# Optimization experiments

Hardware: AMD Instinct MI355X
Metric: run time of the kernel (lower is better)

The kernel has to match this reference:

```python
import math
import jax, jax.numpy as jnp
import numpy as np

BASE = 10000.0
SCALING_FACTOR = 1.0
ORIG_MAX_POS = 4096
BETA_FAST, BETA_SLOW = 32, 1
MSCALE = 0.707
MSCALE_ALL_DIM = 0.707


def _yarn_cos_sin(seq_len: int, dim: int):
    # DeepseekV3YarnRotaryEmbedding._set_cos_sin_cache, computed in numpy (constants)
    def corr_dim(num_rot):
        return dim * math.log(ORIG_MAX_POS / (num_rot * 2 * math.pi)) / (2 * math.log(BASE))
    low = max(math.floor(corr_dim(BETA_FAST)), 0)
    high = min(math.ceil(corr_dim(BETA_SLOW)), dim - 1)
    hi = high + 0.001 if low == high else high
    ramp = np.clip((np.arange(dim // 2, dtype=np.float32) - low) / (hi - low), 0.0, 1.0)
    inv_freq_mask = 1.0 - ramp
    freq_extra = 1.0 / BASE ** (np.arange(0, dim, 2, dtype=np.float32) / dim)
    freq_inter = freq_extra / SCALING_FACTOR
    inv_freq = freq_inter * (1.0 - inv_freq_mask) + freq_extra * inv_freq_mask
    t = np.arange(seq_len, dtype=np.float32)
    freqs = np.outer(t, inv_freq)
    def get_mscale(s, m):
        return 1.0 if s <= 1 else 0.1 * m * math.log(s) + 1.0
    _m = get_mscale(SCALING_FACTOR, MSCALE) / get_mscale(SCALING_FACTOR, MSCALE_ALL_DIM)
    emb = np.concatenate([freqs, freqs], axis=-1)  # [S, dim]
    return jnp.asarray(np.cos(emb) * _m), jnp.asarray(np.sin(emb) * _m)


def _rotate_half(x):
    x1, x2 = jnp.split(x, 2, axis=-1)
    return jnp.concatenate([-x2, x1], axis=-1)


def setup_inputs() -> dict:
    key = jax.random.key(0)
    ks = jax.random.split(key, 5)
    B, S, H, DN, DR, DV = 2, 2048, 16, 128, 64, 128
    return {
        "q_nope": jax.random.normal(ks[0], (B, S, H, DN), jnp.float32),
        "q_pe": jax.random.normal(ks[1], (B, S, H, DR), jnp.float32),
        "k_nope": jax.random.normal(ks[2], (B, S, H, DN), jnp.float32),
        "k_pe": jax.random.normal(ks[3], (B, S, 1, DR), jnp.float32),  # shared rope key head
        "v": jax.random.normal(ks[4], (B, S, H, DV), jnp.float32),
    }


def reference(q_nope, q_pe, k_nope, k_pe, v):
    B, S, H, DN = q_nope.shape
    DR = q_pe.shape[-1]
    sm_scale = (DN + DR) ** (-0.5)  # qk_head_dim**-0.5
    cos, sin = _yarn_cos_sin(S, DR)  # [S, DR]
    cos = cos[None, :, None, :]
    sin = sin[None, :, None, :]
    # decoupled RoPE on the rope slice (apply_rotary_pos_emb with position_ids=arange)
    qp = q_pe * cos + _rotate_half(q_pe) * sin              # [B,S,H,DR]
    kp = k_pe * cos + _rotate_half(k_pe) * sin              # [B,S,1,DR]
    kp = jnp.broadcast_to(kp, (B, S, H, DR))
    q = jnp.concatenate([q_nope, qp], axis=-1)              # [B,S,H,DN+DR]
    k = jnp.concatenate([k_nope, kp], axis=-1)
    # attention_ref: full fp32 logits, causal mask, lse*log2(e), softmax, PV
    logits = jnp.einsum('bmhd,bnhd->bhmn', q.astype(jnp.float32), k.astype(jnp.float32)) * sm_scale
    mask = jnp.arange(S)[:, None] >= jnp.arange(S)[None, :]  # qo_len == kv_len
    logits = jnp.where(mask[None, None], logits, -jnp.inf)
    lse = jnp.transpose(jax.scipy.special.logsumexp(logits, axis=-1), (0, 2, 1)) * math.log2(math.e)
    p = jax.nn.softmax(logits, axis=-1)
    o = jnp.einsum('bhmn,bnhd->bmhd', p, v.astype(jnp.float32))
    o = o.reshape(B * S, H, -1).astype(q_nope.dtype)        # [B*S, H, DV]
    return o, lse
```

## Files before the change

kernel.cpp:

```cpp
#include <hip/hip_runtime.h>
#include <hip/hip_bf16.h>
#include <math.h>

#define NB 2
#define SEQ 2048
#define NH 16
#define DNOPE 128
#define DROT 64
#define DVDIM 128
#define DQK 192
#define BM 64
#define BN 64

typedef __bf16 bf16x8_t __attribute__((ext_vector_type(8)));
typedef float f32x4_t __attribute__((ext_vector_type(4)));

#define LOG2_BASE_OVER_HALFDIM 0.41524101186092028f
#define KSL2 0.10412340175817158f
#define INV_2PI 0.15915494309189535f

typedef __attribute__((address_space(1))) unsigned int as1_uint;
typedef __attribute__((address_space(3))) unsigned int as3_uint;
#define GLOAD16(g, l)                                                        \
  __builtin_amdgcn_global_load_lds((as1_uint*)(g), (as3_uint*)(l), 16, 0, 0)

#define KBF_ELEMS   ((size_t)NB * NH * SEQ * DQK)

#define KN_BLOCKS 4096
#define KR_BLOCKS 128
#define VPREP_BLOCKS 1024

__global__ __launch_bounds__(256) void prep_kernel(
    const float* __restrict__ k_nope, const float* __restrict__ k_pe,
    const float* __restrict__ v, __bf16* __restrict__ Kbf,
    __bf16* __restrict__ Vtb) {
  __shared__ __bf16 T[64][130];
  const int bid = blockIdx.x;
  const int tid = threadIdx.x;
  if (bid < KN_BLOCKS) {
    int gid = bid * 256 + tid;
    int d0 = (gid & 15) * 8;
    int rest = gid >> 4;
    int s = (rest >> 4) & (SEQ - 1);
    int h = rest & (NH - 1);
    int b = rest >> 15;
    const float* p = k_nope + ((size_t)((b * SEQ + s) * NH + h)) * DNOPE + d0;
    float4 a = *(const float4*)p;
    float4 c = *(const float4*)(p + 4);
    bf16x8_t o;
    o[0] = (__bf16)a.x; o[1] = (__bf16)a.y; o[2] = (__bf16)a.z; o[3] = (__bf16)a.w;
    o[4] = (__bf16)c.x; o[5] = (__bf16)c.y; o[6] = (__bf16)c.z; o[7] = (__bf16)c.w;
    *(bf16x8_t*)&Kbf[((size_t)(b * NH + h) * SEQ + s) * DQK + d0] = o;
  } else if (bid < KN_BLOCKS + KR_BLOCKS) {
    int gid = (bid - KN_BLOCKS) * 256 + tid;
    int dr0 = (gid & 7) * 8;
    int rest = gid >> 3;
    int s = rest & (SEQ - 1);
    int b = rest >> 11;
    const float* p = k_pe + (size_t)(b * SEQ + s) * DROT;
    float4 x0 = *(const float4*)(p + dr0);
    float4 x1 = *(const float4*)(p + dr0 + 4);
    int dro = (dr0 < 32) ? dr0 + 32 : dr0 - 32;
    float4 y0 = *(const float4*)(p + dro);
    float4 y1 = *(const float4*)(p + dro + 4);
    float sgn = (dr0 < 32) ? -1.0f : 1.0f;
    float xs[8] = {x0.x, x0.y, x0.z, x0.w, x1.x, x1.y, x1.z, x1.w};
    float ys[8] = {y0.x, y0.y, y0.z, y0.w, y1.x, y1.y, y1.z, y1.w};
    float invf0 = exp2f(-LOG2_BASE_OVER_HALFDIM * (float)(dr0 & 31));
    const float kj[8] = {
      1.0f,
      0.7499083907567589f,
      0.5624875938672282f,
      0.4219181499736729f,
      0.3163923045408737f,
      0.2372497216250197f,
      0.1779391804261401f,
      0.1334543036472316f};
    bf16x8_t o;
#pragma unroll
    for (int j = 0; j < 8; ++j) {
      float rev = (float)s * invf0 * (kj[j] * INV_2PI);
      rev = rev - floorf(rev);
      float sn = __builtin_amdgcn_sinf(rev);
      float cs = __builtin_amdgcn_cosf(rev);
      o[j] = (__bf16)(xs[j] * cs + sgn * ys[j] * sn);
    }
#pragma unroll
    for (int h = 0; h < NH; ++h)
      *(bf16x8_t*)&Kbf[((size_t)(b * NH + h) * SEQ + s) * DQK + DNOPE + dr0] = o;
  } else {
    int vb = bid - KN_BLOCKS - KR_BLOCKS;
    const int s0 = (vb & 31) * 64, h = (vb >> 5) & (NH - 1), b = vb >> 9;
#pragma unroll
    for (int r = 0; r < 8; ++r) {
      int task = tid + r * 256;
      int srow = task >> 5, c4 = (task & 31) * 4;
      const float* p = v + ((size_t)((b * SEQ + s0 + srow) * NH + h)) * DVDIM + c4;
      float4 a = *(const float4*)p;
      T[srow][c4 + 0] = (__bf16)a.x; T[srow][c4 + 1] = (__bf16)a.y;
      T[srow][c4 + 2] = (__bf16)a.z; T[srow][c4 + 3] = (__bf16)a.w;
    }
    __syncthreads();
#pragma unroll
    for (int r = 0; r < 4; ++r) {
      int task = tid + r * 256;
      int dv = task >> 3, c8 = (task & 7) * 8;
      bf16x8_t o;
#pragma unroll
      for (int u = 0; u < 8; ++u) o[u] = T[c8 + u][dv];
      *(bf16x8_t*)&Vtb[((size_t)(b * NH + h) * DVDIM + dv) * SEQ + s0 + c8] = o;
    }
  }
}

__global__ __launch_bounds__(256, 2) void mla_fwd_kernel(
    const float* __restrict__ q_nope, const float* __restrict__ q_pe,
    const __bf16* __restrict__ Kbf, const __bf16* __restrict__ Vtb,
    float* __restrict__ out_o, float* __restrict__ out_lse) {
  __shared__ __bf16 Kl[BN * DQK];
  __shared__ __bf16 Vl0[DVDIM * BN];
  __shared__ __bf16 Vl1[DVDIM * BN];
  __shared__ __bf16 Pl[4 * 16 * BN];

  const int bx = blockIdx.x, h = blockIdx.y, b = blockIdx.z;
  const int tid = threadIdx.x;
  const int w = tid >> 6, lane = tid & 63;
  const int col = lane & 15, quad = lane >> 4;
  const int wm = w & 1;
  const int wnd = w >> 1;
  const int swz = col & 7;
  const int e0 = quad ^ swz, e1 = (quad + 4) ^ swz;
  const int wb = w * 512;

  const __bf16 onev = (col == 0) ? (__bf16)1.0f : (__bf16)0.0f;
  bf16x8_t vxf;
#pragma unroll
  for (int u = 0; u < 8; ++u) vxf[u] = onev;

  const __bf16* Kslab = Kbf + (size_t)(b * NH + h) * SEQ * DQK;
  const __bf16* Vslab = Vtb + (size_t)(b * NH + h) * DVDIM * SEQ;

  int kofs[6];
#pragma unroll
  for (int r = 0; r < 6; ++r) {
    int L = r * 256 + tid;
    int n = L / 24, jj = L - n * 24;
    int jsrc = (jj & ~7) | ((jj & 7) ^ (n & 7));
    kofs[r] = n * DQK + jsrc * 8;
  }
  int vofs[4];
#pragma unroll
  for (int r = 0; r < 4; ++r) {
    int L = r * 256 + tid;
    int dv = L >> 3, jj = L & 7;
    vofs[r] = dv * SEQ + (jj ^ (dv & 7)) * 8;
  }

  for (int half = 0; half < 2; ++half) {
    const int qt = half ? bx : (31 - bx);
    const int qb = qt * BM;

    __syncthreads();
#pragma unroll
    for (int r = 0; r < 6; ++r) GLOAD16(Kslab + kofs[r], &Kl[r * 2048 + wb]);
#pragma unroll
    for (int r = 0; r < 4; ++r) GLOAD16(Vslab + vofs[r], &Vl0[r * 2048 + wb]);

    bf16x8_t qf[2][6];
#pragma unroll
    for (int mt = 0; mt < 2; ++mt) {
      const int mrow = qb + wm * 32 + mt * 16 + col;
      const float* qn = q_nope + (size_t)((b * SEQ + mrow) * NH + h) * DNOPE;
      const float* qp = q_pe   + (size_t)((b * SEQ + mrow) * NH + h) * DROT;
#pragma unroll
      for (int c = 0; c < 4; ++c) {
        const float* p = qn + c * 32 + quad * 8;
        float4 a = *(const float4*)p;
        float4 bq = *(const float4*)(p + 4);
        bf16x8_t f;
        f[0]=(__bf16)(a.x*KSL2);  f[1]=(__bf16)(a.y*KSL2);
        f[2]=(__bf16)(a.z*KSL2);  f[3]=(__bf16)(a.w*KSL2);
        f[4]=(__bf16)(bq.x*KSL2); f[5]=(__bf16)(bq.y*KSL2);
        f[6]=(__bf16)(bq.z*KSL2); f[7]=(__bf16)(bq.w*KSL2);
        qf[mt][c] = f;
      }
      {
        const float* plo = qp + quad * 8;
        const float* phi = qp + 32 + quad * 8;
        float4 lo0 = *(const float4*)plo;
        float4 lo1 = *(const float4*)(plo + 4);
        float4 hi0 = *(const float4*)phi;
        float4 hi1 = *(const float4*)(phi + 4);
        float xl[8] = {lo0.x,lo0.y,lo0.z,lo0.w,lo1.x,lo1.y,lo1.z,lo1.w};
        float xh[8] = {hi0.x,hi0.y,hi0.z,hi0.w,hi1.x,hi1.y,hi1.z,hi1.w};
        bf16x8_t f4v, f5v;
#pragma unroll
        for (int j = 0; j < 8; ++j) {
          int i = quad * 8 + j;
          float invf = exp2f(-LOG2_BASE_OVER_HALFDIM * (float)i);
          float rev = (float)mrow * invf * INV_2PI;
          rev = rev - floorf(rev);
          float sn = __builtin_amdgcn_sinf(rev);
          float cs = __builtin_amdgcn_cosf(rev);
          f4v[j] = (__bf16)((xl[j] * cs - xh[j] * sn) * KSL2);
          f5v[j] = (__bf16)((xh[j] * cs + xl[j] * sn) * KSL2);
        }
        qf[mt][4] = f4v; qf[mt][5] = f5v;
      }
    }

    f32x4_t oacc[2][4];
#pragma unroll
    for (int mt = 0; mt < 2; ++mt)
#pragma unroll
      for (int d = 0; d < 4; ++d) oacc[mt][d] = (f32x4_t){0.f, 0.f, 0.f, 0.f};
    f32x4_t lacc[2];
    lacc[0] = (f32x4_t){0.f, 0.f, 0.f, 0.f};
    lacc[1] = (f32x4_t){0.f, 0.f, 0.f, 0.f};

    auto do_iter = [&](int it, const __bf16* Vcur, __bf16* Vnext) {
      __syncthreads();

      f32x4_t sacc[2][2];
#pragma unroll
      for (int mt = 0; mt < 2; ++mt)
#pragma unroll
        for (int nt = 0; nt < 2; ++nt) sacc[mt][nt] = (f32x4_t){0.f, 0.f, 0.f, 0.f};
#pragma unroll
      for (int nt = 0; nt < 2; ++nt) {
        const __bf16* kr = &Kl[(wnd * 32 + nt * 16 + col) * 24 * 8];
        bf16x8_t kf0 = *(const bf16x8_t*)&kr[e0 * 8];
        bf16x8_t kf1 = *(const bf16x8_t*)&kr[e1 * 8];
        bf16x8_t kf2 = *(const bf16x8_t*)&kr[64 + e0 * 8];
        bf16x8_t kf3 = *(const bf16x8_t*)&kr[64 + e1 * 8];
        bf16x8_t kf4 = *(const bf16x8_t*)&kr[128 + e0 * 8];
        bf16x8_t kf5 = *(const bf16x8_t*)&kr[128 + e1 * 8];
#pragma unroll
        for (int mt = 0; mt < 2; ++mt) {
          sacc[mt][nt] = __builtin_amdgcn_mfma_f32_16x16x32_bf16(qf[mt][0], kf0, sacc[mt][nt], 0, 0, 0);
          sacc[mt][nt] = __builtin_amdgcn_mfma_f32_16x16x32_bf16(qf[mt][1], kf1, sacc[mt][nt], 0, 0, 0);
          sacc[mt][nt] = __builtin_amdgcn_mfma_f32_16x16x32_bf16(qf[mt][2], kf2, sacc[mt][nt], 0, 0, 0);
          sacc[mt][nt] = __builtin_amdgcn_mfma_f32_16x16x32_bf16(qf[mt][3], kf3, sacc[mt][nt], 0, 0, 0);
          sacc[mt][nt] = __builtin_amdgcn_mfma_f32_16x16x32_bf16(qf[mt][4], kf4, sacc[mt][nt], 0, 0, 0);
          sacc[mt][nt] = __builtin_amdgcn_mfma_f32_16x16x32_bf16(qf[mt][5], kf5, sacc[mt][nt], 0, 0, 0);
        }
      }

      const bool dg = (it == qt);
#pragma unroll
      for (int mt = 0; mt < 2; ++mt) {
        __bf16* Pr = &Pl[(wm * 2 + mt) * 16 * BN];
#pragma unroll
        for (int nt = 0; nt < 2; ++nt)
#pragma unroll
          for (int r = 0; r < 4; ++r) {
            float pe = exp2f(sacc[mt][nt][r]);
            if (dg) {
              int nn = (it << 6) + wnd * 32 + nt * 16 + col;
              int mm = qb + wm * 32 + mt * 16 + quad * 4 + r;
              if (nn > mm) pe = 0.0f;
            }
            int row = quad * 4 + r;
            int j = wnd * 4 + nt * 2 + (col >> 3);
            Pr[(row * 8 + (j ^ (row & 7))) * 8 + (col & 7)] = (__bf16)pe;
          }
      }
      __syncthreads();

      if (it < qt) {
        const __bf16* Ksrc = Kslab + (size_t)(it + 1) * BN * DQK;
        const __bf16* Vsrc = Vslab + (it + 1) * BN;
#pragma unroll
        for (int r = 0; r < 6; ++r) GLOAD16(Ksrc + kofs[r], &Kl[r * 2048 + wb]);
#pragma unroll
        for (int r = 0; r < 4; ++r) GLOAD16(Vsrc + vofs[r], &Vnext[r * 2048 + wb]);
      }

      bf16x8_t pf0[2], pf1[2];
#pragma unroll
      for (int mt = 0; mt < 2; ++mt) {
        const __bf16* Pr = &Pl[(wm * 2 + mt) * 16 * BN];
        pf0[mt] = *(const bf16x8_t*)&Pr[(col * 8 + e0) * 8];
        pf1[mt] = *(const bf16x8_t*)&Pr[(col * 8 + e1) * 8];
      }
#pragma unroll
      for (int dt = 0; dt < 4; ++dt) {
        const __bf16* vr = &Vcur[((wnd * 4 + dt) * 16 + col) * 64];
        bf16x8_t vf0 = *(const bf16x8_t*)&vr[e0 * 8];
        bf16x8_t vf1 = *(const bf16x8_t*)&vr[e1 * 8];
#pragma unroll
        for (int mt = 0; mt < 2; ++mt) {
          oacc[mt][dt] = __builtin_amdgcn_mfma_f32_16x16x32_bf16(pf0[mt], vf0, oacc[mt][dt], 0, 0, 0);
          oacc[mt][dt] = __builtin_amdgcn_mfma_f32_16x16x32_bf16(pf1[mt], vf1, oacc[mt][dt], 0, 0, 0);
        }
      }
#pragma unroll
      for (int mt = 0; mt < 2; ++mt) {
        lacc[mt] = __builtin_amdgcn_mfma_f32_16x16x32_bf16(pf0[mt], vxf, lacc[mt], 0, 0, 0);
        lacc[mt] = __builtin_amdgcn_mfma_f32_16x16x32_bf16(pf1[mt], vxf, lacc[mt], 0, 0, 0);
      }
    };

    for (int it = 0; it <= qt; it += 2) {
      do_iter(it, Vl0, Vl1);
      if (it + 1 <= qt) do_iter(it + 1, Vl1, Vl0);
    }

    float lr[2][4], inv_l[2][4];
#pragma unroll
    for (int mt = 0; mt < 2; ++mt)
#pragma unroll
      for (int r = 0; r < 4; ++r) {
        lr[mt][r] = __shfl(lacc[mt][r], lane & 48, 64);
        inv_l[mt][r] = 1.0f / lr[mt][r];
      }
#pragma unroll
    for (int mt = 0; mt < 2; ++mt)
#pragma unroll
      for (int dt = 0; dt < 4; ++dt)
#pragma unroll
        for (int r = 0; r < 4; ++r) {
          int mm = qb + wm * 32 + mt * 16 + quad * 4 + r;
          int dd = wnd * 64 + dt * 16 + col;
          out_o[(size_t)((b * SEQ + mm) * NH + h) * DVDIM + dd] =
              oacc[mt][dt][r] * inv_l[mt][r];
        }
    if (wnd == 0 && col < 4) {
#pragma unroll
      for (int mt = 0; mt < 2; ++mt) {
        int mm = qb + wm * 32 + mt * 16 + quad * 4 + col;
        out_lse[(size_t)(b * SEQ + mm) * NH + h] = log2f(lr[mt][col]);
      }
    }
  }
}

extern "C" void kernel_launch(void* const* d_in, const int* in_sizes, int n_in,
                              void* d_out, int out_size, void* d_ws, size_t ws_size,
                              hipStream_t stream) {
  const float* q_nope = (const float*)d_in[0];
  const float* q_pe   = (const float*)d_in[1];
  const float* k_nope = (const float*)d_in[2];
  const float* k_pe   = (const float*)d_in[3];
  const float* v      = (const float*)d_in[4];
  float* out_o   = (float*)d_out;
  float* out_lse = out_o + (size_t)NB * SEQ * NH * DVDIM;

  __bf16* Kbf = (__bf16*)d_ws;
  __bf16* Vtb = Kbf + KBF_ELEMS;

  prep_kernel<<<dim3(KN_BLOCKS + KR_BLOCKS + VPREP_BLOCKS), dim3(256), 0, stream>>>(
      k_nope, k_pe, v, Kbf, Vtb);
  mla_fwd_kernel<<<dim3(16, NH, NB), dim3(256), 0, stream>>>(
      q_nope, q_pe, Kbf, Vtb, out_o, out_lse);
}
```

Measured before the change: 228.3 us.

## Process both causal query tiles concurrently in one 512-thread block sharing K/V loads

Each block now runs 8 waves: four handle the early query tile and four the late one. Both halves run concurrently over a single K/V sweep, so each K/V tile is loaded into LDS once and used by both query tiles, where before the tiles were handled one after the other. The async global_load_lds double buffer is replaced by register prefetch into a single LDS buffer, with an extra barrier per iteration. Waves on the shorter query tile sit idle at barriers for the remaining iterations, and register pressure rises under the 512-thread launch bound.

```diff
diff --git a/kernel.cpp b/kernel.cpp
--- a/kernel.cpp
+++ b/kernel.cpp
@@ -18,11 +18,6 @@
 #define LOG2_BASE_OVER_HALFDIM 0.41524101186092028f
 #define KSL2 0.10412340175817158f
 #define INV_2PI 0.15915494309189535f
-
-typedef __attribute__((address_space(1))) unsigned int as1_uint;
-typedef __attribute__((address_space(3))) unsigned int as3_uint;
-#define GLOAD16(g, l)                                                        \
-  __builtin_amdgcn_global_load_lds((as1_uint*)(g), (as3_uint*)(l), 16, 0, 0)
 
 #define KBF_ELEMS   ((size_t)NB * NH * SEQ * DQK)
 
@@ -113,24 +108,26 @@
   }
 }
 
-__global__ __launch_bounds__(256, 2) void mla_fwd_kernel(
+__global__ __launch_bounds__(512, 2) void mla_fwd_kernel(
     const float* __restrict__ q_nope, const float* __restrict__ q_pe,
     const __bf16* __restrict__ Kbf, const __bf16* __restrict__ Vtb,
     float* __restrict__ out_o, float* __restrict__ out_lse) {
   __shared__ __bf16 Kl[BN * DQK];
-  __shared__ __bf16 Vl0[DVDIM * BN];
-  __shared__ __bf16 Vl1[DVDIM * BN];
-  __shared__ __bf16 Pl[4 * 16 * BN];
+  __shared__ __bf16 Vl[DVDIM * BN];
+  __shared__ __bf16 Pl[8 * 16 * BN];
 
   const int bx = blockIdx.x, h = blockIdx.y, b = blockIdx.z;
   const int tid = threadIdx.x;
   const int w = tid >> 6, lane = tid & 63;
   const int col = lane & 15, quad = lane >> 4;
-  const int wm = w & 1;
-  const int wnd = w >> 1;
+  const int qh = w >> 2;
+  const int wm = (w >> 1) & 1;
+  const int wnd = w & 1;
+  const int qt = qh ? bx : (31 - bx);
+  const int kmax = 31 - bx;
+  const int qb = qt * BM;
   const int swz = col & 7;
   const int e0 = quad ^ swz, e1 = (quad + 4) ^ swz;
-  const int wb = w * 512;
 
   const __bf16 onev = (col == 0) ? (__bf16)1.0f : (__bf16)0.0f;
   bf16x8_t vxf;
@@ -140,87 +137,98 @@
   const __bf16* Kslab = Kbf + (size_t)(b * NH + h) * SEQ * DQK;
   const __bf16* Vslab = Vtb + (size_t)(b * NH + h) * DVDIM * SEQ;
 
-  int kofs[6];
-#pragma unroll
-  for (int r = 0; r < 6; ++r) {
-    int L = r * 256 + tid;
+  int kofs[3];
+#pragma unroll
+  for (int r = 0; r < 3; ++r) {
+    int L = r * 512 + tid;
     int n = L / 24, jj = L - n * 24;
     int jsrc = (jj & ~7) | ((jj & 7) ^ (n & 7));
     kofs[r] = n * DQK + jsrc * 8;
   }
-  int vofs[4];
-#pragma unroll
-  for (int r = 0; r < 4; ++r) {
-    int L = r * 256 + tid;
+  int vofs[2];
+#pragma unroll
+  for (int r = 0; r < 2; ++r) {
+    int L = r * 512 + tid;
     int dv = L >> 3, jj = L & 7;
     vofs[r] = dv * SEQ + (jj ^ (dv & 7)) * 8;
   }
 
-  for (int half = 0; half < 2; ++half) {
-    const int qt = half ? bx : (31 - bx);
-    const int qb = qt * BM;
-
+  bf16x8_t qf[2][6];
+#pragma unroll
+  for (int mt = 0; mt < 2; ++mt) {
+    const int mrow = qb + wm * 32 + mt * 16 + col;
+    const float* qn = q_nope + (size_t)((b * SEQ + mrow) * NH + h) * DNOPE;
+    const float* qp = q_pe   + (size_t)((b * SEQ + mrow) * NH + h) * DROT;
+#pragma unroll
+    for (int c = 0; c < 4; ++c) {
+      const float* p = qn + c * 32 + quad * 8;
+      float4 a = *(const float4*)p;
+      float4 bq = *(const float4*)(p + 4);
+      bf16x8_t f;
+      f[0]=(__bf16)(a.x*KSL2);  f[1]=(__bf16)(a.y*KSL2);
+      f[2]=(__bf16)(a.z*KSL2);  f[3]=(__bf16)(a.w*KSL2);
+      f[4]=(__bf16)(bq.x*KSL2); f[5]=(__bf16)(bq.y*KSL2);
+      f[6]=(__bf16)(bq.z*KSL2); f[7]=(__bf16)(bq.w*KSL2);
+      qf[mt][c] = f;
+    }
+    {
+      const float* plo = qp + quad * 8;
+      const float* phi = qp + 32 + quad * 8;
+      float4 lo0 = *(const float4*)plo;
+      float4 lo1 = *(const float4*)(plo + 4);
+      float4 hi0 = *(const float4*)phi;
+      float4 hi1 = *(const float4*)(phi + 4);
+      float xl[8] = {lo0.x,lo0.y,lo0.z,lo0.w,lo1.x,lo1.y,lo1.z,lo1.w};
+      float xh[8] = {hi0.x,hi0.y,hi0.z,hi0.w,hi1.x,hi1.y,hi1.z,hi1.w};
+      bf16x8_t f4v, f5v;
+#pragma unroll
+      for (int j = 0; j < 8; ++j) {
+        int i = quad * 8 + j;
+        float invf = exp2f(-LOG2_BASE_OVER_HALFDIM * (float)i);
+        float rev = (float)mrow * invf * INV_2PI;
+        rev = rev - floorf(rev);
+        float sn = __builtin_amdgcn_sinf(rev);
+        float cs = __builtin_amdgcn_cosf(rev);
+        f4v[j] = (__bf16)((xl[j] * cs - xh[j] * sn) * KSL2);
+        f5v[j] = (__bf16)((xh[j] * cs + xl[j] * sn) * KSL2);
+      }
+      qf[mt][4] = f4v; qf[mt][5] = f5v;
+    }
+  }
+
+  f32x4_t oacc[2][4];
+#pragma unroll
+  for (int mt = 0; mt < 2; ++mt)
+#pragma unroll
+    for (int d = 0; d < 4; ++d) oacc[mt][d] = (f32x4_t){0.f, 0.f, 0.f, 0.f};
+  f32x4_t lacc[2];
+  lacc[0] = (f32x4_t){0.f, 0.f, 0.f, 0.f};
+  lacc[1] = (f32x4_t){0.f, 0.f, 0.f, 0.f};
+
+  bf16x8_t Kreg[3], Vreg[2];
+#pragma unroll
+  for (int r = 0; r < 3; ++r) Kreg[r] = *(const bf16x8_t*)(Kslab + kofs[r]);
+#pragma unroll
+  for (int r = 0; r < 2; ++r) Vreg[r] = *(const bf16x8_t*)(Vslab + vofs[r]);
+
+  for (int it = 0; it <= kmax; ++it) {
     __syncthreads();
 #pragma unroll
-    for (int r = 0; r < 6; ++r) GLOAD16(Kslab + kofs[r], &Kl[r * 2048 + wb]);
-#pragma unroll
-    for (int r = 0; r < 4; ++r) GLOAD16(Vslab + vofs[r], &Vl0[r * 2048 + wb]);
-
-    bf16x8_t qf[2][6];
-#pragma unroll
-    for (int mt = 0; mt < 2; ++mt) {
-      const int mrow = qb + wm * 32 + mt * 16 + col;
-      const float* qn = q_nope + (size_t)((b * SEQ + mrow) * NH + h) * DNOPE;
-      const float* qp = q_pe   + (size_t)((b * SEQ + mrow) * NH + h) * DROT;
-#pragma unroll
-      for (int c = 0; c < 4; ++c) {
-        const float* p = qn + c * 32 + quad * 8;
-        float4 a = *(const float4*)p;
-        float4 bq = *(const float4*)(p + 4);
-        bf16x8_t f;
-        f[0]=(__bf16)(a.x*KSL2);  f[1]=(__bf16)(a.y*KSL2);
-        f[2]=(__bf16)(a.z*KSL2);  f[3]=(__bf16)(a.w*KSL2);
-        f[4]=(__bf16)(bq.x*KSL2); f[5]=(__bf16)(bq.y*KSL2);
-        f[6]=(__bf16)(bq.z*KSL2); f[7]=(__bf16)(bq.w*KSL2);
-        qf[mt][c] = f;
-      }
-      {
-        const float* plo = qp + quad * 8;
-        const float* phi = qp + 32 + quad * 8;
-        float4 lo0 = *(const float4*)plo;
-        float4 lo1 = *(const float4*)(plo + 4);
-        float4 hi0 = *(const float4*)phi;
-        float4 hi1 = *(const float4*)(phi + 4);
-        float xl[8] = {lo0.x,lo0.y,lo0.z,lo0.w,lo1.x,lo1.y,lo1.z,lo1.w};
-        float xh[8] = {hi0.x,hi0.y,hi0.z,hi0.w,hi1.x,hi1.y,hi1.z,hi1.w};
-        bf16x8_t f4v, f5v;
-#pragma unroll
-        for (int j = 0; j < 8; ++j) {
-          int i = quad * 8 + j;
-          float invf = exp2f(-LOG2_BASE_OVER_HALFDIM * (float)i);
-          float rev = (float)mrow * invf * INV_2PI;
-          rev = rev - floorf(rev);
-          float sn = __builtin_amdgcn_sinf(rev);
-          float cs = __builtin_amdgcn_cosf(rev);
-          f4v[j] = (__bf16)((xl[j] * cs - xh[j] * sn) * KSL2);
-          f5v[j] = (__bf16)((xh[j] * cs + xl[j] * sn) * KSL2);
-        }
-        qf[mt][4] = f4v; qf[mt][5] = f5v;
-      }
-    }
-
-    f32x4_t oacc[2][4];
-#pragma unroll
-    for (int mt = 0; mt < 2; ++mt)
-#pragma unroll
-      for (int d = 0; d < 4; ++d) oacc[mt][d] = (f32x4_t){0.f, 0.f, 0.f, 0.f};
-    f32x4_t lacc[2];
-    lacc[0] = (f32x4_t){0.f, 0.f, 0.f, 0.f};
-    lacc[1] = (f32x4_t){0.f, 0.f, 0.f, 0.f};
-
-    auto do_iter = [&](int it, const __bf16* Vcur, __bf16* Vnext) {
-      __syncthreads();
-
+    for (int r = 0; r < 3; ++r) *(bf16x8_t*)&Kl[(r * 512 + tid) * 8] = Kreg[r];
+#pragma unroll
+    for (int r = 0; r < 2; ++r) *(bf16x8_t*)&Vl[(r * 512 + tid) * 8] = Vreg[r];
+    __syncthreads();
+    if (it < kmax) {
+      const __bf16* Ksrc = Kslab + (size_t)(it + 1) * BN * DQK;
+      const __bf16* Vsrc = Vslab + (it + 1) * BN;
+#pragma unroll
+      for (int r = 0; r < 3; ++r) Kreg[r] = *(const bf16x8_t*)(Ksrc + kofs[r]);
+#pragma unroll
+      for (int r = 0; r < 2; ++r) Vreg[r] = *(const bf16x8_t*)(Vsrc + vofs[r]);
+    }
+
+    const bool act = (it <= qt);
+    if (act) {
       f32x4_t sacc[2][2];
 #pragma unroll
       for (int mt = 0; mt < 2; ++mt)
@@ -249,7 +257,7 @@
       const bool dg = (it == qt);
 #pragma unroll
       for (int mt = 0; mt < 2; ++mt) {
-        __bf16* Pr = &Pl[(wm * 2 + mt) * 16 * BN];
+        __bf16* Pr = &Pl[(qh * 4 + wm * 2 + mt) * 16 * BN];
 #pragma unroll
         for (int nt = 0; nt < 2; ++nt)
 #pragma unroll
@@ -265,27 +273,20 @@
             Pr[(row * 8 + (j ^ (row & 7))) * 8 + (col & 7)] = (__bf16)pe;
           }
       }
-      __syncthreads();
-
-      if (it < qt) {
-        const __bf16* Ksrc = Kslab + (size_t)(it + 1) * BN * DQK;
-        const __bf16* Vsrc = Vslab + (it + 1) * BN;
-#pragma unroll
-        for (int r = 0; r < 6; ++r) GLOAD16(Ksrc + kofs[r], &Kl[r * 2048 + wb]);
-#pragma unroll
-        for (int r = 0; r < 4; ++r) GLOAD16(Vsrc + vofs[r], &Vnext[r * 2048 + wb]);
-      }
-
+    }
+    __syncthreads();
+
+    if (act) {
       bf16x8_t pf0[2], pf1[2];
 #pragma unroll
       for (int mt = 0; mt < 2; ++mt) {
-        const __bf16* Pr = &Pl[(wm * 2 + mt) * 16 * BN];
+        const __bf16* Pr = &Pl[(qh * 4 + wm * 2 + mt) * 16 * BN];
         pf0[mt] = *(const bf16x8_t*)&Pr[(col * 8 + e0) * 8];
         pf1[mt] = *(const bf16x8_t*)&Pr[(col * 8 + e1) * 8];
       }
 #pragma unroll
       for (int dt = 0; dt < 4; ++dt) {
-        const __bf16* vr = &Vcur[((wnd * 4 + dt) * 16 + col) * 64];
+        const __bf16* vr = &Vl[((wnd * 4 + dt) * 16 + col) * 64];
         bf16x8_t vf0 = *(const bf16x8_t*)&vr[e0 * 8];
         bf16x8_t vf1 = *(const bf16x8_t*)&vr[e1 * 8];
 #pragma unroll
@@ -299,38 +300,33 @@
         lacc[mt] = __builtin_amdgcn_mfma_f32_16x16x32_bf16(pf0[mt], vxf, lacc[mt], 0, 0, 0);
         lacc[mt] = __builtin_amdgcn_mfma_f32_16x16x32_bf16(pf1[mt], vxf, lacc[mt], 0, 0, 0);
       }
-    };
-
-    for (int it = 0; it <= qt; it += 2) {
-      do_iter(it, Vl0, Vl1);
-      if (it + 1 <= qt) do_iter(it + 1, Vl1, Vl0);
-    }
-
-    float lr[2][4], inv_l[2][4];
-#pragma unroll
-    for (int mt = 0; mt < 2; ++mt)
+    }
+  }
+
+  float lr[2][4], inv_l[2][4];
+#pragma unroll
+  for (int mt = 0; mt < 2; ++mt)
+#pragma unroll
+    for (int r = 0; r < 4; ++r) {
+      lr[mt][r] = __shfl(lacc[mt][r], lane & 48, 64);
+      inv_l[mt][r] = 1.0f / lr[mt][r];
+    }
+#pragma unroll
+  for (int mt = 0; mt < 2; ++mt)
+#pragma unroll
+    for (int dt = 0; dt < 4; ++dt)
 #pragma unroll
       for (int r = 0; r < 4; ++r) {
-        lr[mt][r] = __shfl(lacc[mt][r], lane & 48, 64);
-        inv_l[mt][r] = 1.0f / lr[mt][r];
-      }
-#pragma unroll
-    for (int mt = 0; mt < 2; ++mt)
-#pragma unroll
-      for (int dt = 0; dt < 4; ++dt)
-#pragma unroll
-        for (int r = 0; r < 4; ++r) {
-          int mm = qb + wm * 32 + mt * 16 + quad * 4 + r;
-          int dd = wnd * 64 + dt * 16 + col;
-          out_o[(size_t)((b * SEQ + mm) * NH + h) * DVDIM + dd] =
-              oacc[mt][dt][r] * inv_l[mt][r];
-        }
-    if (wnd == 0 && col < 4) {
-#pragma unroll
-      for (int mt = 0; mt < 2; ++mt) {
-        int mm = qb + wm * 32 + mt * 16 + quad * 4 + col;
-        out_lse[(size_t)(b * SEQ + mm) * NH + h] = log2f(lr[mt][col]);
-      }
+        int mm = qb + wm * 32 + mt * 16 + quad * 4 + r;
+        int dd = wnd * 64 + dt * 16 + col;
+        out_o[(size_t)((b * SEQ + mm) * NH + h) * DVDIM + dd] =
+            oacc[mt][dt][r] * inv_l[mt][r];
+      }
+  if (wnd == 0 && col < 4) {
+#pragma unroll
+    for (int mt = 0; mt < 2; ++mt) {
+      int mm = qb + wm * 32 + mt * 16 + quad * 4 + col;
+      out_lse[(size_t)(b * SEQ + mm) * NH + h] = log2f(lr[mt][col]);
     }
   }
 }
@@ -351,6 +347,6 @@
 
   prep_kernel<<<dim3(KN_BLOCKS + KR_BLOCKS + VPREP_BLOCKS), dim3(256), 0, stream>>>(
       k_nope, k_pe, v, Kbf, Vtb);
-  mla_fwd_kernel<<<dim3(16, NH, NB), dim3(256), 0, stream>>>(
+  mla_fwd_kernel<<<dim3(16, NH, NB), dim3(512), 0, stream>>>(
       q_nope, q_pe, Kbf, Vtb, out_o, out_lse);
 }
```

Measured after the change: 236.9 us. +3.8%, slower.
